# Kernel optimization log

Hardware: AMD Instinct MI355X
Metric: run time of the kernel (lower is better)

## Reference

```python
import jax, jax.numpy as jnp
import numpy as np

G = 4       # num_groups
EPS = 1e-5  # BatchNorm eps


def setup_inputs() -> dict:
    key = jax.random.key(0)
    ks = jax.random.split(key, 8)
    B, C, T, V, K = 64, 256, 128, 25, 3
    dk = C // (G * 4)  # reduce_ratio=4 -> dk=16, dk*G=64
    return {
        "x": jax.random.normal(ks[0], (B, C, T, V), dtype=jnp.float32),
        "A": jax.random.uniform(ks[1], (K, V, V), dtype=jnp.float32),
        "Wq": jax.random.normal(ks[2], (dk * G, C), dtype=jnp.float32) * 0.05,
        "Wk": jax.random.normal(ks[3], (dk * G, C), dtype=jnp.float32) * 0.05,
        "Wconv": jax.random.normal(ks[4], (K, G, C // G, C // G), dtype=jnp.float32) * 0.05,
        "alpha": jnp.full((1,), 0.1, dtype=jnp.float32),
        "gamma": jax.random.uniform(ks[5], (C,), dtype=jnp.float32) + 0.5,
        "beta": jax.random.normal(ks[6], (C,), dtype=jnp.float32) * 0.1,
        "running_mean": jnp.zeros((C,), dtype=jnp.float32),
        "running_var": jnp.ones((C,), dtype=jnp.float32),
    }


def reference(x, A, Wq, Wk, Wconv, alpha, gamma, beta, running_mean, running_var):
    B, C, T, V = x.shape
    K = A.shape[0]
    dk = Wq.shape[0] // G
    Cg = C // G

    # Row-normalized fixed adjacency subsets (done in torch __init__)
    A_norm = A / jnp.clip(A.sum(-1, keepdims=True), 1e-6)  # (K,V,V)

    # Q/K 1x1 convs, temporal mean, per-group attention over joints
    q = jnp.einsum('oc,bctv->bov', Wq, x) / T  # conv then mean over T
    k = jnp.einsum('oc,bctv->bov', Wk, x) / T
    q = q.reshape(B, G, dk, V)
    k = k.reshape(B, G, dk, V)
    A_dyn = jnp.einsum('bgdv,bgdw->bgvw', q, k) / jnp.sqrt(jnp.float32(dk))
    A_dyn = jax.nn.softmax(A_dyn, axis=-1).mean(axis=1)  # (B,V,V)

    al = jnp.tanh(alpha[0])
    out = jnp.zeros_like(x)
    for k_idx in range(K):
        A_k = A_norm[k_idx][None] + al * A_dyn               # (B,V,V)
        x_agg = jnp.einsum('bvw,bctw->bctv', A_k, x)         # spatial aggregation
        xg = x_agg.reshape(B, G, Cg, T, V)
        y = jnp.einsum('goc,bgctv->bgotv', Wconv[k_idx], xg).reshape(B, C, T, V)
        out = out + y

    # BatchNorm2d in eval mode (running stats)
    inv = gamma / jnp.sqrt(running_var + EPS)
    bn = out * inv[None, :, None, None] + (beta - running_mean * inv)[None, :, None, None]
    return x + bn
```

## Files before the change

kernel.cpp:

```cpp
#include <hip/hip_runtime.h>

typedef __bf16 bf16x8 __attribute__((ext_vector_type(8)));
typedef __bf16 bf16x4 __attribute__((ext_vector_type(4)));
typedef float  f32x4  __attribute__((ext_vector_type(4)));


__global__ __launch_bounds__(256)
void k_tmean(const float* __restrict__ x, float* __restrict__ xm)
{
    const int bid = blockIdx.x;
    const int b = bid >> 7, c2 = bid & 127;
    const int tid = threadIdx.x;
    const int c_loc = tid >> 7, t = tid & 127;
    const int c = c2 * 2 + c_loc;
    const float* p = x + ((size_t)(b * 256 + c) * 128 + t) * 25;
    float v[25];
#pragma unroll
    for (int j = 0; j < 25; ++j) v[j] = p[j];
#pragma unroll
    for (int s = 1; s < 64; s <<= 1) {
#pragma unroll
        for (int j = 0; j < 25; ++j) v[j] += __shfl_xor(v[j], s);
    }
    __shared__ float part[4][25];
    if ((tid & 63) == 0) {
#pragma unroll
        for (int j = 0; j < 25; ++j) part[tid >> 6][j] = v[j];
    }
    __syncthreads();
    if (tid < 50) {
        const int cl = tid / 25, j = tid - cl * 25;
        xm[((size_t)(b * 256) + c2 * 2 + cl) * 25 + j] =
            (part[cl * 2][j] + part[cl * 2 + 1][j]) * (1.0f / 128.0f);
    }
}

__global__ __launch_bounds__(256)
void k_adyn(const float* __restrict__ xm, const float* __restrict__ A,
            const float* __restrict__ Wq, const float* __restrict__ Wk,
            const float* __restrict__ alpha, __bf16* __restrict__ afull)
{
    const int b = blockIdx.x, tid = threadIdx.x;
    __shared__ float xm_s[256 * 25];
    __shared__ float q_s[64 * 25];
    __shared__ float k_s[64 * 25];
    __shared__ float sm_s[4][25][25];
    __shared__ float ad_s[25][25];
    __shared__ float rs_s[3][25];

    for (int i = tid; i < 256 * 25; i += 256) xm_s[i] = xm[(size_t)b * 6400 + i];
    for (int i = tid; i < 75; i += 256) {
        int k3 = i / 25, v = i - (i / 25) * 25;
        float s = 0.f;
        for (int w = 0; w < 25; ++w) s += A[(k3 * 25 + v) * 25 + w];
        rs_s[k3][v] = fmaxf(s, 1e-6f);
    }
    __syncthreads();

    for (int i = tid; i < 1600; i += 256) {
        int o = i / 25, v = i - o * 25;
        const float* wq = Wq + o * 256;
        const float* wk = Wk + o * 256;
        float aq = 0.f, ak = 0.f;
        for (int c = 0; c < 256; ++c) {
            float xv = xm_s[c * 25 + v];
            aq += wq[c] * xv;
            ak += wk[c] * xv;
        }
        q_s[i] = aq; k_s[i] = ak;
    }
    __syncthreads();

    if (tid < 100) {
        int g = tid / 25, v = tid - (tid / 25) * 25;
        float l[25];
#pragma unroll
        for (int w = 0; w < 25; ++w) {
            float s = 0.f;
#pragma unroll
            for (int d = 0; d < 16; ++d)
                s += q_s[(g * 16 + d) * 25 + v] * k_s[(g * 16 + d) * 25 + w];
            l[w] = s * 0.25f;
        }
        float mx = l[0];
#pragma unroll
        for (int w = 1; w < 25; ++w) mx = fmaxf(mx, l[w]);
        float den = 0.f;
#pragma unroll
        for (int w = 0; w < 25; ++w) { l[w] = expf(l[w] - mx); den += l[w]; }
        float rden = 1.f / den;
#pragma unroll
        for (int w = 0; w < 25; ++w) sm_s[g][v][w] = l[w] * rden;
    }
    __syncthreads();
    for (int i = tid; i < 625; i += 256) {
        int v = i / 25, w = i - (i / 25) * 25;
        ad_s[v][w] = 0.25f * (sm_s[0][v][w] + sm_s[1][v][w] + sm_s[2][v][w] + sm_s[3][v][w]);
    }
    __syncthreads();

    const float al = tanhf(alpha[0]);
    for (int i = tid; i < 3 * 32 * 32; i += 256) {
        int k3 = i >> 10, rem = i & 1023, v = rem >> 5, w = rem & 31;
        float val = 0.f;
        if (v < 25 && w < 25)
            val = A[(k3 * 25 + v) * 25 + w] / rs_s[k3][v] + al * ad_s[v][w];
        afull[(size_t)b * 3072 + i] = (__bf16)val;
    }
}

__global__ __launch_bounds__(256, 4)
void k_main(const float* __restrict__ x, const float* __restrict__ Wconv,
            const __bf16* __restrict__ afull,
            const float* __restrict__ gamma, const float* __restrict__ beta,
            const float* __restrict__ rmean, const float* __restrict__ rvar,
            float* __restrict__ out)
{
    const int bid = blockIdx.x;
    const int tt = bid & 31;
    const int g  = (bid >> 5) & 3;
    const int b  = bid >> 7;
    const int tid = threadIdx.x;
    const int wave = tid >> 6;
    const int lane = tid & 63;
    const int l15 = lane & 15;
    const int lg  = lane >> 4;

    __shared__ __bf16 xs[64 * 4 * 32];
    __shared__ __bf16 xagg[112 * 64];

    {
        const int c = tid >> 2, t = tid & 3;
        const float* p = x + ((size_t)(b * 256 + g * 64 + c) * 128 + tt * 4 + t) * 25;
        float r[25];
#pragma unroll
        for (int j = 0; j < 25; ++j) r[j] = p[j];
        const int rowg = (c * 4 + t) << 2;
        const int sw = c & 7;
#pragma unroll
        for (int ch = 0; ch < 4; ++ch) {
            bf16x8 h;
#pragma unroll
            for (int e = 0; e < 8; ++e) {
                const int v = ch * 8 + e;
                h[e] = (v < 25) ? (__bf16)r[v] : (__bf16)0.f;
            }
            *(bf16x8*)((char*)xs + (((rowg | ch) ^ sw) << 4)) = h;
        }
    }

    bf16x8 bAf[3][2];
#pragma unroll
    for (int k3 = 0; k3 < 3; ++k3)
#pragma unroll
        for (int n = 0; n < 2; ++n)
            bAf[k3][n] = *(const bf16x8*)(afull + ((size_t)(b * 3 + k3) << 10) +
                                          (n * 16 + l15) * 32 + lg * 8);

    const int o_lane = (wave << 4) + l15;
    f32x4 wff[4];
    {
        const float* wp = Wconv + (size_t)((0 * 4 + g) * 64 + o_lane) * 64 + lg * 8;
        wff[0] = *(const f32x4*)wp;        wff[1] = *(const f32x4*)(wp + 4);
        wff[2] = *(const f32x4*)(wp + 32); wff[3] = *(const f32x4*)(wp + 36);
    }

    const int ch = g * 64 + o_lane;
    const float inv  = gamma[ch] / sqrtf(rvar[ch] + 1e-5f);
    const float bias = beta[ch] - rmean[ch] * inv;

    __syncthreads();

    bf16x8 xfrag[4];
#pragma unroll
    for (int m = 0; m < 4; ++m) {
        const int c = m * 16 + l15;
        xfrag[m] = *(const bf16x8*)((char*)xs +
                      (((((c * 4 + wave) << 2) | lg) ^ (c & 7)) << 4));
    }

    f32x4 acc[7];
#pragma unroll
    for (int i = 0; i < 7; ++i) acc[i] = (f32x4){0.f, 0.f, 0.f, 0.f};
    const f32x4 zero4 = {0.f, 0.f, 0.f, 0.f};
    bf16x8 wfc[2];

#pragma unroll
    for (int k3 = 0; k3 < 3; ++k3) {
#pragma unroll
        for (int ks = 0; ks < 2; ++ks) {
            bf16x8 h;
#pragma unroll
            for (int e = 0; e < 4; ++e) {
                h[e]     = (__bf16)wff[ks * 2][e];
                h[e + 4] = (__bf16)wff[ks * 2 + 1][e];
            }
            wfc[ks] = h;
        }
        if (k3 < 2) {
            const float* wp = Wconv + (size_t)(((k3 + 1) * 4 + g) * 64 + o_lane) * 64 + lg * 8;
            wff[0] = *(const f32x4*)wp;        wff[1] = *(const f32x4*)(wp + 4);
            wff[2] = *(const f32x4*)(wp + 32); wff[3] = *(const f32x4*)(wp + 36);
        }

#pragma unroll
        for (int m = 0; m < 4; ++m) {
#pragma unroll
            for (int n = 0; n < 2; ++n) {
                f32x4 d = __builtin_amdgcn_mfma_f32_16x16x32_bf16(xfrag[m], bAf[k3][n],
                                                                  zero4, 0, 0, 0);
                const int v = n * 16 + l15;
                if (v < 25) {
                    const int cc  = wave * 25 + v;
                    const int col = (m * 16 + lg * 4) ^ ((cc & 7) << 3);
                    bf16x4 h;
                    h[0] = (__bf16)d[0]; h[1] = (__bf16)d[1];
                    h[2] = (__bf16)d[2]; h[3] = (__bf16)d[3];
                    *(bf16x4*)((char*)xagg + cc * 128 + col * 2) = h;
                }
            }
        }
        __syncthreads();

#pragma unroll
        for (int mcc = 0; mcc < 7; ++mcc) {
            const int cc = mcc * 16 + l15;
            const int sw2 = (cc & 7) << 3;
#pragma unroll
            for (int ks = 0; ks < 2; ++ks) {
                const int col = (ks * 32 + lg * 8) ^ sw2;
                bf16x8 aF = *(const bf16x8*)((char*)xagg + cc * 128 + col * 2);
                acc[mcc] = __builtin_amdgcn_mfma_f32_16x16x32_bf16(aF, wfc[ks],
                                                                   acc[mcc], 0, 0, 0);
            }
        }
        if (k3 < 2) __syncthreads();
    }

    const size_t obase = (size_t)(b * 256 + ch) * 3200 + tt * 100;
#pragma unroll
    for (int mcc = 0; mcc < 7; ++mcc) {
        const int cc0 = mcc * 16 + lg * 4;
        if (cc0 < 100) {
            f32x4 o4;
#pragma unroll
            for (int j = 0; j < 4; ++j) {
                const int cc = cc0 + j;
                const int t = cc / 25, v = cc - t * 25;
                const int gr = (((o_lane * 4 + t) << 2) | (v >> 3)) ^ (o_lane & 7);
                const float xr = (float)*(const __bf16*)((char*)xs + (gr << 4) + ((v & 7) << 1));
                o4[j] = xr + acc[mcc][j] * inv + bias;
            }
            *(f32x4*)(out + obase + cc0) = o4;
        }
    }
}

extern "C" void kernel_launch(void* const* d_in, const int* in_sizes, int n_in,
                              void* d_out, int out_size, void* d_ws, size_t ws_size,
                              hipStream_t stream) {
    const float* x     = (const float*)d_in[0];
    const float* A     = (const float*)d_in[1];
    const float* Wq    = (const float*)d_in[2];
    const float* Wk    = (const float*)d_in[3];
    const float* Wconv = (const float*)d_in[4];
    const float* alpha = (const float*)d_in[5];
    const float* gamma = (const float*)d_in[6];
    const float* beta  = (const float*)d_in[7];
    const float* rmean = (const float*)d_in[8];
    const float* rvar  = (const float*)d_in[9];
    float* out = (float*)d_out;

    float*  xm    = (float*)d_ws;
    __bf16* afull = (__bf16*)((char*)d_ws + 1638400);

    k_tmean<<<64 * 128, 256, 0, stream>>>(x, xm);
    k_adyn<<<64, 256, 0, stream>>>(xm, A, Wq, Wk, alpha, afull);
    k_main<<<64 * 4 * 32, 256, 0, stream>>>(x, Wconv, afull, gamma, beta, rmean, rvar, out);
}
```

Measured before the change: 235.8 us.

## Pre-convert x to padded bf16 in tmean pass and feed main kernel from it

The temporal-mean kernel now reads x with vectorized loads and also writes a padded bf16 copy of x (32 joints per row). The main kernel loads its MFMA operands directly from that copy, uses Wconv pre-converted to bf16 (done in k_adyn), and double-buffers the adjacency and weight fragments across the three subsets. The aim is to cut fp32 reads and conversion work in the main kernel, at the cost of a 128MB workspace write. The residual add now reads the bf16 copy of x, which loses precision. The old path is kept as a fallback when the workspace is too small.

```diff
diff --git a/kernel.cpp b/kernel.cpp
--- a/kernel.cpp
+++ b/kernel.cpp
@@ -5,40 +5,65 @@
 typedef float  f32x4  __attribute__((ext_vector_type(4)));
 
 
-__global__ __launch_bounds__(256)
-void k_tmean(const float* __restrict__ x, float* __restrict__ xm)
+
+__global__ __launch_bounds__(256, 6)
+void k_tmean_fast(const float* __restrict__ x, float* __restrict__ xm,
+                  __bf16* __restrict__ xpad)
 {
     const int bid = blockIdx.x;
-    const int b = bid >> 7, c2 = bid & 127;
+    const int b = bid >> 5, c8 = bid & 31;
     const int tid = threadIdx.x;
-    const int c_loc = tid >> 7, t = tid & 127;
-    const int c = c2 * 2 + c_loc;
-    const float* p = x + ((size_t)(b * 256 + c) * 128 + t) * 25;
-    float v[25];
-#pragma unroll
-    for (int j = 0; j < 25; ++j) v[j] = p[j];
-#pragma unroll
-    for (int s = 1; s < 64; s <<= 1) {
-#pragma unroll
-        for (int j = 0; j < 25; ++j) v[j] += __shfl_xor(v[j], s);
-    }
-    __shared__ float part[4][25];
-    if ((tid & 63) == 0) {
-#pragma unroll
-        for (int j = 0; j < 25; ++j) part[tid >> 6][j] = v[j];
-    }
-    __syncthreads();
-    if (tid < 50) {
-        const int cl = tid / 25, j = tid - cl * 25;
-        xm[((size_t)(b * 256) + c2 * 2 + cl) * 25 + j] =
-            (part[cl * 2][j] + part[cl * 2 + 1][j]) * (1.0f / 128.0f);
+    const int lane = tid & 63, half = lane >> 5, l32 = lane & 31;
+    const int c = c8 * 8 + (tid >> 6) * 2 + half;
+    const float* base = x + (size_t)(b * 256 + c) * 3200 + l32 * 100;
+    __bf16* xpb = xpad + ((size_t)(b * 256 + c) * 128 + l32 * 4) * 32;
+
+    float acc[25];
+#pragma unroll
+    for (int j = 0; j < 25; ++j) acc[j] = 0.f;
+    f32x4 vv[25];
+
+#pragma unroll
+    for (int dt = 0; dt < 4; ++dt) {
+        const int i_lo = (dt == 0) ? 0 : 6 * dt + 1;
+#pragma unroll
+        for (int i = i_lo; i <= 6 * dt + 6; ++i) {
+            vv[i] = *(const f32x4*)(base + i * 4);
+#pragma unroll
+            for (int e = 0; e < 4; ++e) acc[(4 * i + e) % 25] += vv[i][e];
+        }
+#pragma unroll
+        for (int q = 0; q < 4; ++q) {
+            bf16x8 h;
+#pragma unroll
+            for (int e2 = 0; e2 < 8; ++e2) {
+                const int v = q * 8 + e2;
+                if (v < 25) { const int f = dt * 25 + v; h[e2] = (__bf16)vv[f >> 2][f & 3]; }
+                else        h[e2] = (__bf16)0.f;
+            }
+            *(bf16x8*)(xpb + dt * 32 + q * 8) = h;
+        }
+    }
+
+    __shared__ float part[256][26];
+#pragma unroll
+    for (int j = 0; j < 25; ++j) part[tid][j] = acc[j];
+    __syncthreads();
+    if (tid < 200) {
+        const int cl = tid / 25, v = tid - cl * 25;
+        const int src = (cl >> 1) * 64 + (cl & 1) * 32;
+        float s = 0.f;
+#pragma unroll
+        for (int k = 0; k < 32; ++k) s += part[src + k][v];
+        xm[((size_t)(b * 256) + c8 * 8 + cl) * 25 + v] = s * (1.0f / 128.0f);
     }
 }
 
 __global__ __launch_bounds__(256)
 void k_adyn(const float* __restrict__ xm, const float* __restrict__ A,
             const float* __restrict__ Wq, const float* __restrict__ Wk,
-            const float* __restrict__ alpha, __bf16* __restrict__ afull)
+            const float* __restrict__ alpha, __bf16* __restrict__ afull,
+            const float* __restrict__ Wconv, __bf16* __restrict__ wcb)
 {
     const int b = blockIdx.x, tid = threadIdx.x;
     __shared__ float xm_s[256 * 25];
@@ -47,6 +72,9 @@
     __shared__ float sm_s[4][25][25];
     __shared__ float ad_s[25][25];
     __shared__ float rs_s[3][25];
+
+    for (int i = tid; i < 768; i += 256)
+        wcb[b * 768 + i] = (__bf16)Wconv[b * 768 + i];
 
     for (int i = tid; i < 256 * 25; i += 256) xm_s[i] = xm[(size_t)b * 6400 + i];
     for (int i = tid; i < 75; i += 256) {
@@ -109,12 +137,148 @@
     }
 }
 
+__global__ __launch_bounds__(256, 5)
+void k_main_fast(const __bf16* __restrict__ xpad, const __bf16* __restrict__ wcb,
+                 const __bf16* __restrict__ afull,
+                 const float* __restrict__ gamma, const float* __restrict__ beta,
+                 const float* __restrict__ rmean, const float* __restrict__ rvar,
+                 float* __restrict__ out)
+{
+    const int bid = blockIdx.x;
+    const int tt = bid & 31;
+    const int g  = (bid >> 5) & 3;
+    const int b  = bid >> 7;
+    const int tid = threadIdx.x;
+    const int wave = tid >> 6, lane = tid & 63, l15 = lane & 15, lg = lane >> 4;
+
+    __shared__ __bf16 xagg[112 * 64];
+
+    const __bf16* xp = xpad + ((size_t)((b * 256 + g * 64) * 128) + tt * 4 + wave) * 32;
+    bf16x8 xfrag[4];
+#pragma unroll
+    for (int m = 0; m < 4; ++m)
+        xfrag[m] = *(const bf16x8*)(xp + (size_t)(m * 16 + l15) * 4096 + lg * 8);
+
+    const int o_lane = (wave << 4) + l15;
+    const int ch = (g << 6) + o_lane;
+    const float inv  = gamma[ch] / sqrtf(rvar[ch] + 1e-5f);
+    const float bias = beta[ch] - rmean[ch] * inv;
+
+    const __bf16* ab = afull + ((size_t)(b * 3) << 10) + l15 * 32 + lg * 8;
+    const __bf16* wb = wcb + (size_t)(g * 64 + o_lane) * 64 + lg * 8;
+    bf16x8 bAc[2], bAn[2], wfc[2], wfn[2];
+    bAn[0] = *(const bf16x8*)(ab);
+    bAn[1] = *(const bf16x8*)(ab + 16 * 32);
+    wfn[0] = *(const bf16x8*)(wb);
+    wfn[1] = *(const bf16x8*)(wb + 32);
+
+    f32x4 acc[7];
+#pragma unroll
+    for (int i = 0; i < 7; ++i) acc[i] = (f32x4){0.f, 0.f, 0.f, 0.f};
+    const f32x4 zero4 = {0.f, 0.f, 0.f, 0.f};
+
+#pragma unroll
+    for (int k3 = 0; k3 < 3; ++k3) {
+        bAc[0] = bAn[0]; bAc[1] = bAn[1];
+        wfc[0] = wfn[0]; wfc[1] = wfn[1];
+        if (k3 < 2) {
+            const __bf16* ab2 = ab + (size_t)(k3 + 1) * 1024;
+            bAn[0] = *(const bf16x8*)(ab2);
+            bAn[1] = *(const bf16x8*)(ab2 + 16 * 32);
+            const __bf16* wb2 = wb + (size_t)(k3 + 1) * 16384;
+            wfn[0] = *(const bf16x8*)(wb2);
+            wfn[1] = *(const bf16x8*)(wb2 + 32);
+        }
+        if (k3 > 0) __syncthreads();
+
+#pragma unroll
+        for (int m = 0; m < 4; ++m) {
+#pragma unroll
+            for (int n = 0; n < 2; ++n) {
+                f32x4 d = __builtin_amdgcn_mfma_f32_16x16x32_bf16(xfrag[m], bAc[n],
+                                                                  zero4, 0, 0, 0);
+                const int v = n * 16 + l15;
+                if (v < 25) {
+                    const int cc  = wave * 25 + v;
+                    const int col = (m * 16 + lg * 4) ^ ((cc & 7) << 3);
+                    bf16x4 h;
+                    h[0] = (__bf16)d[0]; h[1] = (__bf16)d[1];
+                    h[2] = (__bf16)d[2]; h[3] = (__bf16)d[3];
+                    *(bf16x4*)((char*)xagg + cc * 128 + col * 2) = h;
+                }
+            }
+        }
+        __syncthreads();
+
+#pragma unroll
+        for (int mcc = 0; mcc < 7; ++mcc) {
+            const int cc = mcc * 16 + l15;
+            const int sw2 = (cc & 7) << 3;
+#pragma unroll
+            for (int ks = 0; ks < 2; ++ks) {
+                const int col = (ks * 32 + lg * 8) ^ sw2;
+                bf16x8 aF = *(const bf16x8*)((char*)xagg + cc * 128 + col * 2);
+                acc[mcc] = __builtin_amdgcn_mfma_f32_16x16x32_bf16(aF, wfc[ks],
+                                                                   acc[mcc], 0, 0, 0);
+            }
+        }
+    }
+
+    const __bf16* xr = xpad + ((size_t)(b * 256 + ch) * 128 + tt * 4) * 32;
+    float* op = out + (size_t)(b * 256 + ch) * 3200 + tt * 100;
+#pragma unroll
+    for (int mcc = 0; mcc < 7; ++mcc) {
+        const int cc0 = (mcc << 4) + (lg << 2);
+        if (cc0 < 100) {
+            f32x4 o4;
+#pragma unroll
+            for (int j = 0; j < 4; ++j) {
+                const int cc = cc0 + j;
+                const int t = cc / 25, v = cc - t * 25;
+                o4[j] = (float)xr[t * 32 + v] + acc[mcc][j] * inv + bias;
+            }
+            *(f32x4*)(op + cc0) = o4;
+        }
+    }
+}
+
+
+__global__ __launch_bounds__(256)
+void k_tmean_slow(const float* __restrict__ x, float* __restrict__ xm)
+{
+    const int bid = blockIdx.x;
+    const int b = bid >> 7, c2 = bid & 127;
+    const int tid = threadIdx.x;
+    const int c_loc = tid >> 7, t = tid & 127;
+    const int c = c2 * 2 + c_loc;
+    const float* p = x + ((size_t)(b * 256 + c) * 128 + t) * 25;
+    float v[25];
+#pragma unroll
+    for (int j = 0; j < 25; ++j) v[j] = p[j];
+#pragma unroll
+    for (int s = 1; s < 64; s <<= 1) {
+#pragma unroll
+        for (int j = 0; j < 25; ++j) v[j] += __shfl_xor(v[j], s);
+    }
+    __shared__ float part[4][25];
+    if ((tid & 63) == 0) {
+#pragma unroll
+        for (int j = 0; j < 25; ++j) part[tid >> 6][j] = v[j];
+    }
+    __syncthreads();
+    if (tid < 50) {
+        const int cl = tid / 25, j = tid - cl * 25;
+        xm[((size_t)(b * 256) + c2 * 2 + cl) * 25 + j] =
+            (part[cl * 2][j] + part[cl * 2 + 1][j]) * (1.0f / 128.0f);
+    }
+}
+
 __global__ __launch_bounds__(256, 4)
-void k_main(const float* __restrict__ x, const float* __restrict__ Wconv,
-            const __bf16* __restrict__ afull,
-            const float* __restrict__ gamma, const float* __restrict__ beta,
-            const float* __restrict__ rmean, const float* __restrict__ rvar,
-            float* __restrict__ out)
+void k_main_slow(const float* __restrict__ x, const float* __restrict__ Wconv,
+                 const __bf16* __restrict__ afull,
+                 const float* __restrict__ gamma, const float* __restrict__ beta,
+                 const float* __restrict__ rmean, const float* __restrict__ rvar,
+                 float* __restrict__ out)
 {
     const int bid = blockIdx.x;
     const int tt = bid & 31;
@@ -273,8 +437,19 @@
 
     float*  xm    = (float*)d_ws;
     __bf16* afull = (__bf16*)((char*)d_ws + 1638400);
-
-    k_tmean<<<64 * 128, 256, 0, stream>>>(x, xm);
-    k_adyn<<<64, 256, 0, stream>>>(xm, A, Wq, Wk, alpha, afull);
-    k_main<<<64 * 4 * 32, 256, 0, stream>>>(x, Wconv, afull, gamma, beta, rmean, rvar, out);
-}
+    __bf16* wcb   = (__bf16*)((char*)d_ws + 2031616);
+    __bf16* xpad  = (__bf16*)((char*)d_ws + 2129920);
+
+    const size_t need = 2129920ull + 134217728ull;
+    if (ws_size >= need) {
+        k_tmean_fast<<<64 * 32, 256, 0, stream>>>(x, xm, xpad);
+        k_adyn<<<64, 256, 0, stream>>>(xm, A, Wq, Wk, alpha, afull, Wconv, wcb);
+        k_main_fast<<<64 * 4 * 32, 256, 0, stream>>>(xpad, wcb, afull, gamma, beta,
+                                                     rmean, rvar, out);
+    } else {
+        k_tmean_slow<<<64 * 128, 256, 0, stream>>>(x, xm);
+        k_adyn<<<64, 256, 0, stream>>>(xm, A, Wq, Wk, alpha, afull, Wconv, wcb);
+        k_main_slow<<<64 * 4 * 32, 256, 0, stream>>>(x, Wconv, afull, gamma, beta,
+                                                     rmean, rvar, out);
+    }
+}
```

New measurement: 406.8 us. 72.5% more time.

## Emit padded bf16 copy of x in tmean pass and feed main kernel from it

Applied to the files above, without the earlier changes.

The temporal-mean kernel now stages x through shared memory with coalesced vector loads and also writes a padded bf16 copy of x (32 joints per row). The adyn kernel pre-converts Wconv to bf16. The main kernel reads MFMA fragments and the residual directly from the bf16 copy instead of converting fp32 x through shared memory. This removes the fp32 re-read of x and the per-block conversion, but adds a bf16 write and read of a tensor about 64% the size of x. The residual add now uses the bf16-rounded x.

```diff
diff --git a/kernel.cpp b/kernel.cpp
--- a/kernel.cpp
+++ b/kernel.cpp
@@ -6,17 +6,41 @@
 
 
 __global__ __launch_bounds__(256)
-void k_tmean(const float* __restrict__ x, float* __restrict__ xm)
+void k_tmean2(const float* __restrict__ x, float* __restrict__ xm,
+              __bf16* __restrict__ xpad)
 {
     const int bid = blockIdx.x;
     const int b = bid >> 7, c2 = bid & 127;
+    const int c0 = c2 * 2;
     const int tid = threadIdx.x;
+
+    __shared__ float xls[6400];
+    const float* gx = x + (size_t)(b * 256 + c0) * 3200;
+#pragma unroll
+    for (int i = 0; i < 7; ++i) {
+        const int idx = i * 256 + tid;
+        if (idx < 1600)
+            *(f32x4*)(&xls[idx * 4]) = *(const f32x4*)(gx + idx * 4);
+    }
+    __syncthreads();
+
     const int c_loc = tid >> 7, t = tid & 127;
-    const int c = c2 * 2 + c_loc;
-    const float* p = x + ((size_t)(b * 256 + c) * 128 + t) * 25;
     float v[25];
 #pragma unroll
-    for (int j = 0; j < 25; ++j) v[j] = p[j];
+    for (int j = 0; j < 25; ++j) v[j] = xls[c_loc * 3200 + t * 25 + j];
+
+    __bf16* xpb = xpad + ((size_t)(b * 256 + c0 + c_loc) * 128 + t) * 32;
+#pragma unroll
+    for (int q = 0; q < 4; ++q) {
+        bf16x8 h;
+#pragma unroll
+        for (int e = 0; e < 8; ++e) {
+            const int ve = q * 8 + e;
+            h[e] = (ve < 25) ? (__bf16)v[ve] : (__bf16)0.f;
+        }
+        *(bf16x8*)(xpb + q * 8) = h;
+    }
+
 #pragma unroll
     for (int s = 1; s < 64; s <<= 1) {
 #pragma unroll
@@ -24,13 +48,14 @@
     }
     __shared__ float part[4][25];
     if ((tid & 63) == 0) {
-#pragma unroll
-        for (int j = 0; j < 25; ++j) part[tid >> 6][j] = v[j];
+        const int w = tid >> 6;
+#pragma unroll
+        for (int j = 0; j < 25; ++j) part[w][j] = v[j];
     }
     __syncthreads();
     if (tid < 50) {
         const int cl = tid / 25, j = tid - cl * 25;
-        xm[((size_t)(b * 256) + c2 * 2 + cl) * 25 + j] =
+        xm[((size_t)(b * 256) + c0 + cl) * 25 + j] =
             (part[cl * 2][j] + part[cl * 2 + 1][j]) * (1.0f / 128.0f);
     }
 }
@@ -38,7 +63,8 @@
 __global__ __launch_bounds__(256)
 void k_adyn(const float* __restrict__ xm, const float* __restrict__ A,
             const float* __restrict__ Wq, const float* __restrict__ Wk,
-            const float* __restrict__ alpha, __bf16* __restrict__ afull)
+            const float* __restrict__ alpha, __bf16* __restrict__ afull,
+            const float* __restrict__ Wconv, __bf16* __restrict__ wcb)
 {
     const int b = blockIdx.x, tid = threadIdx.x;
     __shared__ float xm_s[256 * 25];
@@ -47,6 +73,9 @@
     __shared__ float sm_s[4][25][25];
     __shared__ float ad_s[25][25];
     __shared__ float rs_s[3][25];
+
+    for (int i = tid; i < 768; i += 256)
+        wcb[b * 768 + i] = (__bf16)Wconv[b * 768 + i];
 
     for (int i = tid; i < 256 * 25; i += 256) xm_s[i] = xm[(size_t)b * 6400 + i];
     for (int i = tid; i < 75; i += 256) {
@@ -110,104 +139,55 @@
 }
 
 __global__ __launch_bounds__(256, 4)
-void k_main(const float* __restrict__ x, const float* __restrict__ Wconv,
-            const __bf16* __restrict__ afull,
-            const float* __restrict__ gamma, const float* __restrict__ beta,
-            const float* __restrict__ rmean, const float* __restrict__ rvar,
-            float* __restrict__ out)
+void k_main2(const __bf16* __restrict__ xpad, const __bf16* __restrict__ wcb,
+             const __bf16* __restrict__ afull,
+             const float* __restrict__ gamma, const float* __restrict__ beta,
+             const float* __restrict__ rmean, const float* __restrict__ rvar,
+             float* __restrict__ out)
 {
     const int bid = blockIdx.x;
     const int tt = bid & 31;
     const int g  = (bid >> 5) & 3;
     const int b  = bid >> 7;
     const int tid = threadIdx.x;
-    const int wave = tid >> 6;
-    const int lane = tid & 63;
-    const int l15 = lane & 15;
-    const int lg  = lane >> 4;
-
-    __shared__ __bf16 xs[64 * 4 * 32];
+    const int wave = tid >> 6, lane = tid & 63, l15 = lane & 15, lg = lane >> 4;
+
     __shared__ __bf16 xagg[112 * 64];
 
-    {
-        const int c = tid >> 2, t = tid & 3;
-        const float* p = x + ((size_t)(b * 256 + g * 64 + c) * 128 + tt * 4 + t) * 25;
-        float r[25];
-#pragma unroll
-        for (int j = 0; j < 25; ++j) r[j] = p[j];
-        const int rowg = (c * 4 + t) << 2;
-        const int sw = c & 7;
-#pragma unroll
-        for (int ch = 0; ch < 4; ++ch) {
-            bf16x8 h;
-#pragma unroll
-            for (int e = 0; e < 8; ++e) {
-                const int v = ch * 8 + e;
-                h[e] = (v < 25) ? (__bf16)r[v] : (__bf16)0.f;
-            }
-            *(bf16x8*)((char*)xs + (((rowg | ch) ^ sw) << 4)) = h;
-        }
-    }
-
-    bf16x8 bAf[3][2];
-#pragma unroll
-    for (int k3 = 0; k3 < 3; ++k3)
-#pragma unroll
-        for (int n = 0; n < 2; ++n)
-            bAf[k3][n] = *(const bf16x8*)(afull + ((size_t)(b * 3 + k3) << 10) +
-                                          (n * 16 + l15) * 32 + lg * 8);
+    const __bf16* xp = xpad + ((size_t)((b * 256 + g * 64) * 128) + tt * 4 + wave) * 32;
+    bf16x8 xfrag[4];
+#pragma unroll
+    for (int m = 0; m < 4; ++m)
+        xfrag[m] = *(const bf16x8*)(xp + (size_t)(m * 16 + l15) * 4096 + lg * 8);
 
     const int o_lane = (wave << 4) + l15;
-    f32x4 wff[4];
-    {
-        const float* wp = Wconv + (size_t)((0 * 4 + g) * 64 + o_lane) * 64 + lg * 8;
-        wff[0] = *(const f32x4*)wp;        wff[1] = *(const f32x4*)(wp + 4);
-        wff[2] = *(const f32x4*)(wp + 32); wff[3] = *(const f32x4*)(wp + 36);
-    }
-
-    const int ch = g * 64 + o_lane;
+    const int ch = (g << 6) + o_lane;
     const float inv  = gamma[ch] / sqrtf(rvar[ch] + 1e-5f);
     const float bias = beta[ch] - rmean[ch] * inv;
 
-    __syncthreads();
-
-    bf16x8 xfrag[4];
-#pragma unroll
-    for (int m = 0; m < 4; ++m) {
-        const int c = m * 16 + l15;
-        xfrag[m] = *(const bf16x8*)((char*)xs +
-                      (((((c * 4 + wave) << 2) | lg) ^ (c & 7)) << 4));
-    }
+    const __bf16* ab = afull + ((size_t)(b * 3) << 10) + l15 * 32 + lg * 8;
+    const __bf16* wb = wcb + (size_t)(g * 64 + o_lane) * 64 + lg * 8;
 
     f32x4 acc[7];
 #pragma unroll
     for (int i = 0; i < 7; ++i) acc[i] = (f32x4){0.f, 0.f, 0.f, 0.f};
     const f32x4 zero4 = {0.f, 0.f, 0.f, 0.f};
-    bf16x8 wfc[2];
 
 #pragma unroll
     for (int k3 = 0; k3 < 3; ++k3) {
-#pragma unroll
-        for (int ks = 0; ks < 2; ++ks) {
-            bf16x8 h;
-#pragma unroll
-            for (int e = 0; e < 4; ++e) {
-                h[e]     = (__bf16)wff[ks * 2][e];
-                h[e + 4] = (__bf16)wff[ks * 2 + 1][e];
-            }
-            wfc[ks] = h;
-        }
-        if (k3 < 2) {
-            const float* wp = Wconv + (size_t)(((k3 + 1) * 4 + g) * 64 + o_lane) * 64 + lg * 8;
-            wff[0] = *(const f32x4*)wp;        wff[1] = *(const f32x4*)(wp + 4);
-            wff[2] = *(const f32x4*)(wp + 32); wff[3] = *(const f32x4*)(wp + 36);
-        }
+        bf16x8 bA[2], wf[2];
+        bA[0] = *(const bf16x8*)(ab + (size_t)k3 * 1024);
+        bA[1] = *(const bf16x8*)(ab + (size_t)k3 * 1024 + 16 * 32);
+        wf[0] = *(const bf16x8*)(wb + (size_t)k3 * 16384);
+        wf[1] = *(const bf16x8*)(wb + (size_t)k3 * 16384 + 32);
+
+        if (k3 > 0) __syncthreads();
 
 #pragma unroll
         for (int m = 0; m < 4; ++m) {
 #pragma unroll
             for (int n = 0; n < 2; ++n) {
-                f32x4 d = __builtin_amdgcn_mfma_f32_16x16x32_bf16(xfrag[m], bAf[k3][n],
+                f32x4 d = __builtin_amdgcn_mfma_f32_16x16x32_bf16(xfrag[m], bA[n],
                                                                   zero4, 0, 0, 0);
                 const int v = n * 16 + l15;
                 if (v < 25) {
@@ -230,28 +210,26 @@
             for (int ks = 0; ks < 2; ++ks) {
                 const int col = (ks * 32 + lg * 8) ^ sw2;
                 bf16x8 aF = *(const bf16x8*)((char*)xagg + cc * 128 + col * 2);
-                acc[mcc] = __builtin_amdgcn_mfma_f32_16x16x32_bf16(aF, wfc[ks],
+                acc[mcc] = __builtin_amdgcn_mfma_f32_16x16x32_bf16(aF, wf[ks],
                                                                    acc[mcc], 0, 0, 0);
             }
         }
-        if (k3 < 2) __syncthreads();
-    }
-
-    const size_t obase = (size_t)(b * 256 + ch) * 3200 + tt * 100;
+    }
+
+    const __bf16* xr = xpad + ((size_t)(b * 256 + ch) * 128 + tt * 4) * 32;
+    float* op = out + (size_t)(b * 256 + ch) * 3200 + tt * 100;
 #pragma unroll
     for (int mcc = 0; mcc < 7; ++mcc) {
-        const int cc0 = mcc * 16 + lg * 4;
+        const int cc0 = (mcc << 4) + (lg << 2);
         if (cc0 < 100) {
             f32x4 o4;
 #pragma unroll
             for (int j = 0; j < 4; ++j) {
                 const int cc = cc0 + j;
                 const int t = cc / 25, v = cc - t * 25;
-                const int gr = (((o_lane * 4 + t) << 2) | (v >> 3)) ^ (o_lane & 7);
-                const float xr = (float)*(const __bf16*)((char*)xs + (gr << 4) + ((v & 7) << 1));
-                o4[j] = xr + acc[mcc][j] * inv + bias;
+                o4[j] = (float)xr[t * 32 + v] + acc[mcc][j] * inv + bias;
             }
-            *(f32x4*)(out + obase + cc0) = o4;
+            *(f32x4*)(op + cc0) = o4;
         }
     }
 }
@@ -273,8 +251,11 @@
 
     float*  xm    = (float*)d_ws;
     __bf16* afull = (__bf16*)((char*)d_ws + 1638400);
-
-    k_tmean<<<64 * 128, 256, 0, stream>>>(x, xm);
-    k_adyn<<<64, 256, 0, stream>>>(xm, A, Wq, Wk, alpha, afull);
-    k_main<<<64 * 4 * 32, 256, 0, stream>>>(x, Wconv, afull, gamma, beta, rmean, rvar, out);
-}
+    __bf16* wcb   = (__bf16*)((char*)d_ws + 2031616);
+    __bf16* xpad  = (__bf16*)((char*)d_ws + 2129920);
+
+    k_tmean2<<<64 * 128, 256, 0, stream>>>(x, xm, xpad);
+    k_adyn<<<64, 256, 0, stream>>>(xm, A, Wq, Wk, alpha, afull, Wconv, wcb);
+    k_main2<<<64 * 4 * 32, 256, 0, stream>>>(xpad, wcb, afull, gamma, beta,
+                                             rmean, rvar, out);
+}
```

New measurement: 299.5 us. 1.27x slower.
